# Optimization experiments

Measured on AMD Instinct MI355X. Metric: run time of the kernel, lower is better.

The kernel has to match this reference:

```python
import jax, jax.numpy as jnp
import numpy as np

N = 50000        # num nodes
E = 800000       # num edges (avg degree 16)
IN_DIM = 64
OUT_DIM = 64
PE_DIM = 24
HEADS = 2
HID = OUT_DIM * HEADS  # 128


def setup_inputs() -> dict:
    key = jax.random.key(0)
    ks = jax.random.split(key, 16)
    std = 0.1  # trunc_normal_(std=0.1) init in the torch module
    return {
        "x": jax.random.normal(ks[0], (N, IN_DIM), jnp.float32),
        "pe_index": jax.random.randint(ks[1], (2, E), 0, N, jnp.int32),
        "pe_val": jax.random.normal(ks[2], (E, PE_DIM), jnp.float32),
        # edge-weight MLP (blocks): input proj, one residual FFN block, final proj
        "W_in": jax.random.normal(ks[3], (PE_DIM, HID), jnp.float32) * std,
        "b_in": jnp.zeros((HID,), jnp.float32),
        "W1": jax.random.normal(ks[4], (HID, HID), jnp.float32) * std,
        "b1": jnp.zeros((HID,), jnp.float32),
        "W2": jax.random.normal(ks[5], (HID, HID), jnp.float32) * std,
        "b2": jnp.zeros((HID,), jnp.float32),
        "W_fin": jax.random.normal(ks[6], (HID, HID), jnp.float32) * std,
        "b_fin": jnp.zeros((HID,), jnp.float32),
        # node feature -> multi-head projection
        "W_x": jax.random.normal(ks[7], (IN_DIM, HID), jnp.float32) * std,
        "b_x": jnp.zeros((HID,), jnp.float32),
        # per-head output bias
        "head_bias": jnp.zeros((1, HEADS, OUT_DIM), jnp.float32),
        # final out projection
        "W_out": jax.random.normal(ks[8], (HID, OUT_DIM), jnp.float32) * std,
        "b_out": jnp.zeros((OUT_DIM,), jnp.float32),
    }


def _edge_mlp(pe, W_in, b_in, W1, b1, W2, b2, W_fin, b_fin):
    # Linear(pe_dim->hid), then residual block [GELU, Linear, GELU, Linear, +res], then Linear(hid->hid)
    g = lambda t: jax.nn.gelu(t, approximate=False)  # torch nn.GELU default = exact erf
    x0 = pe @ W_in + b_in                     # [E, HID]
    h = g(x0) @ W1 + b1
    h = g(h) @ W2 + b2
    x0 = h + x0                               # ResidualLayer: x + x_res
    return x0 @ W_fin + b_fin                 # [E, HID]


def reference(x, pe_index, pe_val, W_in, b_in, W1, b1, W2, b2, W_fin, b_fin,
              W_x, b_x, head_bias, W_out, b_out):
    tgt = pe_index[0]  # messages aggregate to edge_index[0]
    src = pe_index[1]
    score = _edge_mlp(pe_val, W_in, b_in, W1, b1, W2, b2, W_fin, b_fin)
    score = score.reshape(-1, HEADS, OUT_DIM)                 # [E, H, D]
    xh = (x @ W_x + b_x).reshape(-1, HEADS, OUT_DIM)          # [N, H, D]
    msg = xh[src] * score                                     # gather-multiply
    wV = jax.ops.segment_sum(msg, tgt, num_segments=N)        # scatter-add [N, H, D]
    deg = jax.ops.segment_sum(jnp.ones((msg.shape[0],), jnp.float32), tgt, num_segments=N)
    wV = wV / jnp.maximum(deg, 1.0)[:, None, None]            # average=True -> mean aggregation
    h = (wV + head_bias).reshape(-1, HEADS * OUT_DIM)
    return h @ W_out + b_out                                  # out_proj: [N, OUT_DIM]
```

## Files before the change

### kernel.cpp

```cpp
#include <hip/hip_runtime.h>
#include <hip/hip_bf16.h>
#include <math.h>

#define NN 50000
#define EE 800000
#define HID 128
#define PED 24
#define IND 64
#define OUTD 64
#define EBLK 128
#define AKS 136

typedef short bf16x8 __attribute__((ext_vector_type(8)));
typedef float f32x4 __attribute__((ext_vector_type(4)));

__device__ __forceinline__ float gelu_fast(float x) {
    float x2 = x * x;
    float t = __builtin_fmaf(x2, -0.07135481627f, -1.5957691216f);
    float e = __expf(x * t);
    return x * __builtin_amdgcn_rcpf(1.0f + e);
}
__device__ __forceinline__ unsigned short f2bf(float f) {
    unsigned int u = __float_as_uint(f);
    u = (u + 0x7fffu + ((u >> 16) & 1u)) >> 16;
    return (unsigned short)u;
}
__device__ __forceinline__ unsigned int pkbf2(float a, float b) {
    __hip_bfloat162 h = __float22bfloat162_rn(make_float2(a, b));
    return *reinterpret_cast<unsigned int*>(&h);
}
__device__ __forceinline__ float bf2f(unsigned short u) {
    return __uint_as_float((unsigned int)u << 16);
}

__global__ __launch_bounds__(256) void pre_kernel(
    const float* __restrict__ x, const float* __restrict__ W_x,
    const float* __restrict__ b_x, unsigned short* __restrict__ xhb,
    const float* __restrict__ W_in, const float* __restrict__ W1,
    const float* __restrict__ W2, const float* __restrict__ Wf,
    unsigned short* __restrict__ WT_in, unsigned short* __restrict__ WT1,
    unsigned short* __restrict__ WT2, unsigned short* __restrict__ WTf,
    float* __restrict__ wV, int* __restrict__ cnt) {
    int bx = blockIdx.x;
    if (bx < 6250) {
        int gid = bx * 256 + threadIdx.x;
        int n = gid >> 5;
        int q = gid & 31;
        *(float4*)&wV[(size_t)n * HID + q * 4] = make_float4(0.f, 0.f, 0.f, 0.f);
        const float* xr = x + (size_t)n * IND;
        float4 acc = *(const float4*)&b_x[q * 4];
#pragma unroll 8
        for (int k = 0; k < IND; k++) {
            float xk = xr[k];
            float4 w = *(const float4*)&W_x[k * HID + q * 4];
            acc.x += xk * w.x; acc.y += xk * w.y;
            acc.z += xk * w.z; acc.w += xk * w.w;
        }
        uint2 p;
        p.x = pkbf2(acc.x, acc.y);
        p.y = pkbf2(acc.z, acc.w);
        ((uint2*)&xhb[(size_t)n * HID])[q] = p;
    } else {
        int idx = (bx - 6250) * 256 + threadIdx.x;
        if (idx < NN) cnt[idx] = 0;
        if (idx < 4096) {
            int j = idx >> 5, k = idx & 31;
            WT_in[idx] = f2bf(k < PED ? W_in[k * HID + j] : 0.f);
        } else if (idx < 4096 + 16384) {
            int i = idx - 4096; int j = i >> 7, k = i & 127;
            WT1[i] = f2bf(W1[k * HID + j]);
        } else if (idx < 4096 + 32768) {
            int i = idx - 4096 - 16384; int j = i >> 7, k = i & 127;
            WT2[i] = f2bf(W2[k * HID + j]);
        } else if (idx < 4096 + 49152) {
            int i = idx - 4096 - 32768; int j = i >> 7, k = i & 127;
            WTf[i] = f2bf(Wf[k * HID + j]);
        }
    }
}

__global__ __launch_bounds__(256) void hist_kernel(const int* __restrict__ pe_idx,
                                                   int* __restrict__ cnt) {
    int e = blockIdx.x * 256 + threadIdx.x;
    if (e < EE) atomicAdd(&cnt[pe_idx[e]], 1);
}

__global__ __launch_bounds__(1024) void scan_kernel(const int* __restrict__ cnt,
                                                    int* __restrict__ woff) {
    __shared__ int s_w[16];
    int tid = threadIdx.x;
    const int chunk = (NN + 1023) / 1024;
    int base = tid * chunk;
    int end = base + chunk; if (end > NN) end = NN;
    int s = 0;
    for (int i = base; i < end; i++) s += cnt[i];
    int v = s;
    int lane = tid & 63, wid = tid >> 6;
#pragma unroll
    for (int d = 1; d < 64; d <<= 1) {
        int u = __shfl_up(v, d, 64);
        if (lane >= d) v += u;
    }
    if (lane == 63) s_w[wid] = v;
    __syncthreads();
    if (tid < 16) {
        int wv = s_w[tid];
#pragma unroll
        for (int d = 1; d < 16; d <<= 1) {
            int u = __shfl_up(wv, d, 64);
            if (tid >= d) wv += u;
        }
        s_w[tid] = wv;
    }
    __syncthreads();
    int exc = v - s + (wid ? s_w[wid - 1] : 0);
    int run = exc;
    for (int i = base; i < end; i++) { woff[i] = run; run += cnt[i]; }
}

__global__ __launch_bounds__(256) void scatter_kernel(const int* __restrict__ pe_idx,
                                                      int* __restrict__ woff,
                                                      int* __restrict__ perm) {
    int e = blockIdx.x * 256 + threadIdx.x;
    if (e < EE) {
        int t = pe_idx[e];
        int p = atomicAdd(&woff[t], 1);
        perm[p] = e;
    }
}

__global__ __launch_bounds__(512, 4) void edge_kernel(
    const float* __restrict__ pe_val, const int* __restrict__ pe_idx,
    const int* __restrict__ perm, const unsigned short* __restrict__ xhb,
    const unsigned short* __restrict__ WT_in, const unsigned short* __restrict__ WT1,
    const unsigned short* __restrict__ WT2, const unsigned short* __restrict__ WTf,
    const float* __restrict__ b_in, const float* __restrict__ b1,
    const float* __restrict__ b2, const float* __restrict__ bfin,
    float* __restrict__ wV) {
    __shared__ __align__(16) unsigned short s_act[2][EBLK][AKS];
    __shared__ int s_tgt[EBLK], s_src[EBLK];

    const int tid = threadIdx.x;
    const int lane = tid & 63;
    const int w = tid >> 6;
    const int cg = w & 3;
    const int eh = w >> 2;
    const int ebase = eh * 64;
    const int l15 = lane & 15;
    const int quad = lane >> 4;
    const long b0 = (long)blockIdx.x * EBLK;

    if (tid < EBLK) {
        int eid = perm[b0 + tid];
        s_tgt[tid] = pe_idx[eid];
        s_src[tid] = pe_idx[EE + eid];
    }
#pragma unroll
    for (int i = 0; i < 4; i++) {
        int idx = tid + i * 512; int e = idx >> 4, k2 = idx & 15;
        float2 v = make_float2(0.f, 0.f);
        if (k2 < 12) {
            int eid = perm[b0 + e];
            v = *(const float2*)&pe_val[(size_t)eid * PED + k2 * 2];
        }
        *(unsigned int*)&s_act[0][e][k2 * 2] = pkbf2(v.x, v.y);
    }
    __syncthreads();

    f32x4 C[2][4];
    f32x4 x0s[2][4];

    {
        float4 ba = *(const float4*)&b_in[(2 * cg + 0) * 16 + quad * 4];
        float4 bb = *(const float4*)&b_in[(2 * cg + 1) * 16 + quad * 4];
        f32x4 ci0 = {ba.x, ba.y, ba.z, ba.w};
        f32x4 ci1 = {bb.x, bb.y, bb.z, bb.w};
        bf16x8 a0 = *(const bf16x8*)&WT_in[((2 * cg + 0) * 16 + l15) * 32 + quad * 8];
        bf16x8 a1 = *(const bf16x8*)&WT_in[((2 * cg + 1) * 16 + l15) * 32 + quad * 8];
#pragma unroll
        for (int u = 0; u < 4; u++) {
            bf16x8 bfr = *(const bf16x8*)&s_act[0][ebase + u * 16 + l15][quad * 8];
            C[0][u] = __builtin_amdgcn_mfma_f32_16x16x32_bf16(a0, bfr, ci0, 0, 0, 0);
            C[1][u] = __builtin_amdgcn_mfma_f32_16x16x32_bf16(a1, bfr, ci1, 0, 0, 0);
        }
    }
#pragma unroll
    for (int t = 0; t < 2; t++) {
        int ch0 = (2 * cg + t) * 16 + quad * 4;
#pragma unroll
        for (int u = 0; u < 4; u++) {
            int e = ebase + u * 16 + l15;
            f32x4 c = C[t][u];
            x0s[t][u] = c;
            uint2 p;
            p.x = pkbf2(gelu_fast(c[0]), gelu_fast(c[1]));
            p.y = pkbf2(gelu_fast(c[2]), gelu_fast(c[3]));
            *(uint2*)&s_act[1][e][ch0] = p;
        }
    }
    __syncthreads();

#define GEMM128(WT, BIAS, SB)                                                  \
    {                                                                          \
        float4 ba_ = *(const float4*)&(BIAS)[(2 * cg + 0) * 16 + quad * 4];    \
        float4 bb_ = *(const float4*)&(BIAS)[(2 * cg + 1) * 16 + quad * 4];    \
        f32x4 ci0 = {ba_.x, ba_.y, ba_.z, ba_.w};                              \
        f32x4 ci1 = {bb_.x, bb_.y, bb_.z, bb_.w};                              \
        _Pragma("unroll") for (int u = 0; u < 4; u++) {                        \
            C[0][u] = ci0; C[1][u] = ci1;                                      \
        }                                                                      \
        _Pragma("unroll") for (int ks = 0; ks < 4; ks++) {                     \
            bf16x8 a0 = *(const bf16x8*)&(WT)[((2 * cg + 0) * 16 + l15) * HID  \
                                              + ks * 32 + quad * 8];           \
            bf16x8 a1 = *(const bf16x8*)&(WT)[((2 * cg + 1) * 16 + l15) * HID  \
                                              + ks * 32 + quad * 8];           \
            _Pragma("unroll") for (int u = 0; u < 4; u++) {                    \
                bf16x8 bfr = *(const bf16x8*)&s_act[SB][ebase + u * 16 + l15]  \
                                                   [ks * 32 + quad * 8];       \
                C[0][u] = __builtin_amdgcn_mfma_f32_16x16x32_bf16(a0, bfr,     \
                                                                  C[0][u], 0, 0, 0); \
                C[1][u] = __builtin_amdgcn_mfma_f32_16x16x32_bf16(a1, bfr,     \
                                                                  C[1][u], 0, 0, 0); \
            }                                                                  \
        }                                                                      \
    }

    GEMM128(WT1, b1, 1);
#pragma unroll
    for (int t = 0; t < 2; t++) {
        int ch0 = (2 * cg + t) * 16 + quad * 4;
#pragma unroll
        for (int u = 0; u < 4; u++) {
            int e = ebase + u * 16 + l15;
            f32x4 c = C[t][u];
            uint2 p;
            p.x = pkbf2(gelu_fast(c[0]), gelu_fast(c[1]));
            p.y = pkbf2(gelu_fast(c[2]), gelu_fast(c[3]));
            *(uint2*)&s_act[0][e][ch0] = p;
        }
    }
    __syncthreads();

    GEMM128(WT2, b2, 0);
#pragma unroll
    for (int t = 0; t < 2; t++) {
        int ch0 = (2 * cg + t) * 16 + quad * 4;
#pragma unroll
        for (int u = 0; u < 4; u++) {
            int e = ebase + u * 16 + l15;
            f32x4 c = C[t][u];
            f32x4 x0 = x0s[t][u];
            uint2 p;
            p.x = pkbf2(c[0] + x0[0], c[1] + x0[1]);
            p.y = pkbf2(c[2] + x0[2], c[3] + x0[3]);
            *(uint2*)&s_act[1][e][ch0] = p;
        }
    }
    __syncthreads();

    GEMM128(WTf, bfin, 1);
#pragma unroll
    for (int t = 0; t < 2; t++) {
        int ch0 = (2 * cg + t) * 16 + quad * 4;
#pragma unroll
        for (int u = 0; u < 4; u++) {
            int e = ebase + u * 16 + l15;
            f32x4 c = C[t][u];
            uint2 p;
            p.x = pkbf2(c[0], c[1]);
            p.y = pkbf2(c[2], c[3]);
            *(uint2*)&s_act[0][e][ch0] = p;
        }
    }
    __syncthreads();

    {
        const int c = tid & 127;
        const int q = tid >> 7;
        const int e0 = q * 32;
        float acc = 0.f;
        int prev = s_tgt[e0];
        bool firstseg = true;
#pragma unroll
        for (int b = 0; b < 4; b++) {
            float xs[8];
#pragma unroll
            for (int j = 0; j < 8; j++) {
                int e = e0 + b * 8 + j;
                xs[j] = bf2f(xhb[(size_t)s_src[e] * HID + c]);
            }
#pragma unroll
            for (int j = 0; j < 8; j++) {
                int e = e0 + b * 8 + j;
                int tg = s_tgt[e];
                if (tg != prev) {
                    if (firstseg) atomicAdd(&wV[(size_t)prev * HID + c], acc);
                    else          wV[(size_t)prev * HID + c] = acc;
                    firstseg = false;
                    acc = 0.f;
                    prev = tg;
                }
                float sc = bf2f(s_act[0][e][c]);
                acc += xs[j] * sc;
            }
        }
        atomicAdd(&wV[(size_t)prev * HID + c], acc);
    }
#undef GEMM128
}

__global__ __launch_bounds__(256) void out_kernel(
    const float* __restrict__ wV, const int* __restrict__ cnt,
    const float* __restrict__ head_bias, const float* __restrict__ W_out,
    const float* __restrict__ b_out, float* __restrict__ out) {
    int gid = blockIdx.x * 256 + threadIdx.x;
    int n = gid >> 4;
    int q = gid & 15;
    if (n >= NN) return;
    float inv = 1.0f / fmaxf((float)cnt[n], 1.0f);
    const float* wr = wV + (size_t)n * HID;
    float4 acc = *(const float4*)&b_out[q * 4];
#pragma unroll 4
    for (int k = 0; k < HID; k++) {
        float hv = wr[k] * inv + head_bias[k];
        float4 wv4 = *(const float4*)&W_out[k * OUTD + q * 4];
        acc.x += hv * wv4.x; acc.y += hv * wv4.y;
        acc.z += hv * wv4.z; acc.w += hv * wv4.w;
    }
    *(float4*)&out[(size_t)n * OUTD + q * 4] = acc;
}

extern "C" void kernel_launch(void* const* d_in, const int* in_sizes, int n_in,
                              void* d_out, int out_size, void* d_ws, size_t ws_size,
                              hipStream_t stream) {
    const float* x      = (const float*)d_in[0];
    const int*   pe_idx = (const int*)d_in[1];
    const float* pe_val = (const float*)d_in[2];
    const float* W_in   = (const float*)d_in[3];
    const float* b_in   = (const float*)d_in[4];
    const float* W1     = (const float*)d_in[5];
    const float* b1     = (const float*)d_in[6];
    const float* W2     = (const float*)d_in[7];
    const float* b2     = (const float*)d_in[8];
    const float* Wf     = (const float*)d_in[9];
    const float* bfin   = (const float*)d_in[10];
    const float* W_x    = (const float*)d_in[11];
    const float* b_x    = (const float*)d_in[12];
    const float* hb     = (const float*)d_in[13];
    const float* W_out  = (const float*)d_in[14];
    const float* b_out  = (const float*)d_in[15];
    float* out = (float*)d_out;

    float* wV   = (float*)d_ws;
    int*   cnt  = (int*)(wV + (size_t)NN * HID);
    int*   woff = cnt + NN;
    int*   perm = woff + NN;
    unsigned short* WT_in = (unsigned short*)(perm + EE);
    unsigned short* WT1   = WT_in + 128 * 32;
    unsigned short* WT2   = WT1 + 128 * 128;
    unsigned short* WTf   = WT2 + 128 * 128;
    unsigned short* xhb   = WTf + 128 * 128;

    pre_kernel<<<6250 + 208, 256, 0, stream>>>(x, W_x, b_x, xhb,
                                               W_in, W1, W2, Wf,
                                               WT_in, WT1, WT2, WTf, wV, cnt);
    hist_kernel<<<(EE + 255) / 256, 256, 0, stream>>>(pe_idx, cnt);
    scan_kernel<<<1, 1024, 0, stream>>>(cnt, woff);
    scatter_kernel<<<(EE + 255) / 256, 256, 0, stream>>>(pe_idx, woff, perm);

    edge_kernel<<<EE / EBLK, 512, 0, stream>>>(pe_val, pe_idx, perm, xhb,
                                               WT_in, WT1, WT2, WTf,
                                               b_in, b1, b2, bfin, wV);

    out_kernel<<<(NN * 16 + 255) / 256, 256, 0, stream>>>(wV, cnt, hb, W_out,
                                                          b_out, out);
}
```

Before: 702.3 us.

## Restructure edge MLP kernel: smaller edge tile, LDS-staged swizzled weights, vectorized scatter

Shrinks the edge tile from 128 to 80 edges and drops the double-buffered padded activation array for a single XOR-swizzled activation buffer. Each 128x128 weight matrix is now staged once into LDS with the same swizzle, so waves read MFMA A fragments from shared memory instead of global memory. The residual x0 is kept packed in bf16, and the xh gathers are issued before the final sync. The scatter step now handles 4 channels per thread with 5 edges per group and always uses atomics. Occupancy is raised to 6 blocks per CU, at the cost of more barriers, more weight-staging traffic per edge, and more atomics per edge.

```diff
diff --git a/kernel.cpp b/kernel.cpp
--- a/kernel.cpp
+++ b/kernel.cpp
@@ -8,8 +8,7 @@
 #define PED 24
 #define IND 64
 #define OUTD 64
-#define EBLK 128
-#define AKS 136
+#define EBLK 80
 
 typedef short bf16x8 __attribute__((ext_vector_type(8)));
 typedef float f32x4 __attribute__((ext_vector_type(4)));
@@ -29,8 +28,11 @@
     __hip_bfloat162 h = __float22bfloat162_rn(make_float2(a, b));
     return *reinterpret_cast<unsigned int*>(&h);
 }
-__device__ __forceinline__ float bf2f(unsigned short u) {
-    return __uint_as_float((unsigned int)u << 16);
+__device__ __forceinline__ float bflo(unsigned int u) {
+    return __uint_as_float(u << 16);
+}
+__device__ __forceinline__ float bfhi(unsigned int u) {
+    return __uint_as_float(u & 0xffff0000u);
 }
 
 __global__ __launch_bounds__(256) void pre_kernel(
@@ -129,7 +131,7 @@
     }
 }
 
-__global__ __launch_bounds__(512, 4) void edge_kernel(
+__global__ __launch_bounds__(512, 6) void edge_kernel(
     const float* __restrict__ pe_val, const int* __restrict__ pe_idx,
     const int* __restrict__ perm, const unsigned short* __restrict__ xhb,
     const unsigned short* __restrict__ WT_in, const unsigned short* __restrict__ WT1,
@@ -137,18 +139,19 @@
     const float* __restrict__ b_in, const float* __restrict__ b1,
     const float* __restrict__ b2, const float* __restrict__ bfin,
     float* __restrict__ wV) {
-    __shared__ __align__(16) unsigned short s_act[2][EBLK][AKS];
+    __shared__ __align__(16) unsigned short s_W[HID * HID];
+    __shared__ __align__(16) unsigned short s_act[EBLK * HID];
     __shared__ int s_tgt[EBLK], s_src[EBLK];
 
     const int tid = threadIdx.x;
     const int lane = tid & 63;
-    const int w = tid >> 6;
-    const int cg = w & 3;
-    const int eh = w >> 2;
-    const int ebase = eh * 64;
+    const int cg = tid >> 6;
     const int l15 = lane & 15;
     const int quad = lane >> 4;
+    const int swz4 = (l15 & 7) << 4;
     const long b0 = (long)blockIdx.x * EBLK;
+    char* actB = (char*)s_act;
+    char* wB = (char*)s_W;
 
     if (tid < EBLK) {
         int eid = perm[b0 + tid];
@@ -157,156 +160,154 @@
     }
 #pragma unroll
     for (int i = 0; i < 4; i++) {
-        int idx = tid + i * 512; int e = idx >> 4, k2 = idx & 15;
-        float2 v = make_float2(0.f, 0.f);
-        if (k2 < 12) {
-            int eid = perm[b0 + e];
-            v = *(const float2*)&pe_val[(size_t)eid * PED + k2 * 2];
-        }
-        *(unsigned int*)&s_act[0][e][k2 * 2] = pkbf2(v.x, v.y);
-    }
-    __syncthreads();
-
-    f32x4 C[2][4];
-    f32x4 x0s[2][4];
+        int idx = tid + i * 512; int r = idx >> 4, seg = idx & 15;
+        *(uint4*)(wB + r * 256 + ((seg * 16) ^ ((r & 7) << 4))) =
+            *(const uint4*)&WT1[r * HID + seg * 8];
+    }
+#pragma unroll
+    for (int i = 0; i < 3; i++) {
+        int idx = tid + i * 512;
+        if (idx < EBLK * 16) {
+            int e = idx >> 4, k2 = idx & 15;
+            float2 v = make_float2(0.f, 0.f);
+            if (k2 < 12) {
+                int eid = perm[b0 + e];
+                v = *(const float2*)&pe_val[(size_t)eid * PED + k2 * 2];
+            }
+            *(unsigned int*)(actB + e * 256 + ((k2 * 4) ^ ((e & 7) << 4))) =
+                pkbf2(v.x, v.y);
+        }
+    }
+    __syncthreads();
+
+    const int ch0 = cg * 16 + quad * 4;
+    f32x4 C[5];
+    unsigned int x0pk[5][2];
 
     {
-        float4 ba = *(const float4*)&b_in[(2 * cg + 0) * 16 + quad * 4];
-        float4 bb = *(const float4*)&b_in[(2 * cg + 1) * 16 + quad * 4];
-        f32x4 ci0 = {ba.x, ba.y, ba.z, ba.w};
-        f32x4 ci1 = {bb.x, bb.y, bb.z, bb.w};
-        bf16x8 a0 = *(const bf16x8*)&WT_in[((2 * cg + 0) * 16 + l15) * 32 + quad * 8];
-        bf16x8 a1 = *(const bf16x8*)&WT_in[((2 * cg + 1) * 16 + l15) * 32 + quad * 8];
-#pragma unroll
-        for (int u = 0; u < 4; u++) {
-            bf16x8 bfr = *(const bf16x8*)&s_act[0][ebase + u * 16 + l15][quad * 8];
-            C[0][u] = __builtin_amdgcn_mfma_f32_16x16x32_bf16(a0, bfr, ci0, 0, 0, 0);
-            C[1][u] = __builtin_amdgcn_mfma_f32_16x16x32_bf16(a1, bfr, ci1, 0, 0, 0);
-        }
-    }
-#pragma unroll
-    for (int t = 0; t < 2; t++) {
-        int ch0 = (2 * cg + t) * 16 + quad * 4;
-#pragma unroll
-        for (int u = 0; u < 4; u++) {
-            int e = ebase + u * 16 + l15;
-            f32x4 c = C[t][u];
-            x0s[t][u] = c;
-            uint2 p;
-            p.x = pkbf2(gelu_fast(c[0]), gelu_fast(c[1]));
-            p.y = pkbf2(gelu_fast(c[2]), gelu_fast(c[3]));
-            *(uint2*)&s_act[1][e][ch0] = p;
-        }
-    }
-    __syncthreads();
-
-#define GEMM128(WT, BIAS, SB)                                                  \
+        float4 bb = *(const float4*)&b_in[ch0];
+        f32x4 ci = {bb.x, bb.y, bb.z, bb.w};
+        bf16x8 a = *(const bf16x8*)&WT_in[(cg * 16 + l15) * 32 + quad * 8];
+#pragma unroll
+        for (int u = 0; u < 5; u++) {
+            bf16x8 bfr = *(const bf16x8*)(actB + (u * 16 + l15) * 256 +
+                                          ((quad * 16) ^ swz4));
+            C[u] = __builtin_amdgcn_mfma_f32_16x16x32_bf16(a, bfr, ci, 0, 0, 0);
+        }
+    }
+    __syncthreads();
+#pragma unroll
+    for (int u = 0; u < 5; u++) {
+        int e = u * 16 + l15;
+        f32x4 c = C[u];
+        x0pk[u][0] = pkbf2(c[0], c[1]);
+        x0pk[u][1] = pkbf2(c[2], c[3]);
+        uint2 p;
+        p.x = pkbf2(gelu_fast(c[0]), gelu_fast(c[1]));
+        p.y = pkbf2(gelu_fast(c[2]), gelu_fast(c[3]));
+        *(uint2*)(actB + e * 256 + ((ch0 * 2) ^ swz4)) = p;
+    }
+    __syncthreads();
+
+#define GEMM128(BIAS)                                                          \
     {                                                                          \
-        float4 ba_ = *(const float4*)&(BIAS)[(2 * cg + 0) * 16 + quad * 4];    \
-        float4 bb_ = *(const float4*)&(BIAS)[(2 * cg + 1) * 16 + quad * 4];    \
-        f32x4 ci0 = {ba_.x, ba_.y, ba_.z, ba_.w};                              \
-        f32x4 ci1 = {bb_.x, bb_.y, bb_.z, bb_.w};                              \
-        _Pragma("unroll") for (int u = 0; u < 4; u++) {                        \
-            C[0][u] = ci0; C[1][u] = ci1;                                      \
-        }                                                                      \
+        float4 bb_ = *(const float4*)&(BIAS)[ch0];                             \
+        f32x4 ci = {bb_.x, bb_.y, bb_.z, bb_.w};                               \
+        _Pragma("unroll") for (int u = 0; u < 5; u++) C[u] = ci;               \
         _Pragma("unroll") for (int ks = 0; ks < 4; ks++) {                     \
-            bf16x8 a0 = *(const bf16x8*)&(WT)[((2 * cg + 0) * 16 + l15) * HID  \
-                                              + ks * 32 + quad * 8];           \
-            bf16x8 a1 = *(const bf16x8*)&(WT)[((2 * cg + 1) * 16 + l15) * HID  \
-                                              + ks * 32 + quad * 8];           \
-            _Pragma("unroll") for (int u = 0; u < 4; u++) {                    \
-                bf16x8 bfr = *(const bf16x8*)&s_act[SB][ebase + u * 16 + l15]  \
-                                                   [ks * 32 + quad * 8];       \
-                C[0][u] = __builtin_amdgcn_mfma_f32_16x16x32_bf16(a0, bfr,     \
-                                                                  C[0][u], 0, 0, 0); \
-                C[1][u] = __builtin_amdgcn_mfma_f32_16x16x32_bf16(a1, bfr,     \
-                                                                  C[1][u], 0, 0, 0); \
+            bf16x8 a = *(const bf16x8*)(wB + (cg * 16 + l15) * 256 +           \
+                                        ((ks * 64 + quad * 16) ^ swz4));       \
+            _Pragma("unroll") for (int u = 0; u < 5; u++) {                    \
+                bf16x8 bfr = *(const bf16x8*)(actB + (u * 16 + l15) * 256 +    \
+                                              ((ks * 64 + quad * 16) ^ swz4)); \
+                C[u] = __builtin_amdgcn_mfma_f32_16x16x32_bf16(a, bfr, C[u],   \
+                                                               0, 0, 0);       \
             }                                                                  \
         }                                                                      \
     }
 
-    GEMM128(WT1, b1, 1);
-#pragma unroll
-    for (int t = 0; t < 2; t++) {
-        int ch0 = (2 * cg + t) * 16 + quad * 4;
-#pragma unroll
-        for (int u = 0; u < 4; u++) {
-            int e = ebase + u * 16 + l15;
-            f32x4 c = C[t][u];
-            uint2 p;
-            p.x = pkbf2(gelu_fast(c[0]), gelu_fast(c[1]));
-            p.y = pkbf2(gelu_fast(c[2]), gelu_fast(c[3]));
-            *(uint2*)&s_act[0][e][ch0] = p;
-        }
-    }
-    __syncthreads();
-
-    GEMM128(WT2, b2, 0);
-#pragma unroll
-    for (int t = 0; t < 2; t++) {
-        int ch0 = (2 * cg + t) * 16 + quad * 4;
-#pragma unroll
-        for (int u = 0; u < 4; u++) {
-            int e = ebase + u * 16 + l15;
-            f32x4 c = C[t][u];
-            f32x4 x0 = x0s[t][u];
-            uint2 p;
-            p.x = pkbf2(c[0] + x0[0], c[1] + x0[1]);
-            p.y = pkbf2(c[2] + x0[2], c[3] + x0[3]);
-            *(uint2*)&s_act[1][e][ch0] = p;
-        }
-    }
-    __syncthreads();
-
-    GEMM128(WTf, bfin, 1);
-#pragma unroll
-    for (int t = 0; t < 2; t++) {
-        int ch0 = (2 * cg + t) * 16 + quad * 4;
-#pragma unroll
-        for (int u = 0; u < 4; u++) {
-            int e = ebase + u * 16 + l15;
-            f32x4 c = C[t][u];
-            uint2 p;
-            p.x = pkbf2(c[0], c[1]);
-            p.y = pkbf2(c[2], c[3]);
-            *(uint2*)&s_act[0][e][ch0] = p;
-        }
+#define STAGE_W(WT)                                                            \
+    _Pragma("unroll") for (int i = 0; i < 4; i++) {                            \
+        int idx = tid + i * 512; int r = idx >> 4, seg = idx & 15;             \
+        *(uint4*)(wB + r * 256 + ((seg * 16) ^ ((r & 7) << 4))) =              \
+            *(const uint4*)&(WT)[r * HID + seg * 8];                           \
+    }
+
+    GEMM128(b1);
+    __syncthreads();
+#pragma unroll
+    for (int u = 0; u < 5; u++) {
+        int e = u * 16 + l15;
+        f32x4 c = C[u];
+        uint2 p;
+        p.x = pkbf2(gelu_fast(c[0]), gelu_fast(c[1]));
+        p.y = pkbf2(gelu_fast(c[2]), gelu_fast(c[3]));
+        *(uint2*)(actB + e * 256 + ((ch0 * 2) ^ swz4)) = p;
+    }
+    STAGE_W(WT2);
+    __syncthreads();
+
+    GEMM128(b2);
+    __syncthreads();
+#pragma unroll
+    for (int u = 0; u < 5; u++) {
+        int e = u * 16 + l15;
+        f32x4 c = C[u];
+        uint2 p;
+        p.x = pkbf2(c[0] + bflo(x0pk[u][0]), c[1] + bfhi(x0pk[u][0]));
+        p.y = pkbf2(c[2] + bflo(x0pk[u][1]), c[3] + bfhi(x0pk[u][1]));
+        *(uint2*)(actB + e * 256 + ((ch0 * 2) ^ swz4)) = p;
+    }
+    STAGE_W(WTf);
+    __syncthreads();
+
+    GEMM128(bfin);
+    const int g = tid >> 5;
+    const int c4w = tid & 31;
+    uint2 xv[5];
+#pragma unroll
+    for (int j = 0; j < 5; j++) {
+        xv[j] = *(const uint2*)&xhb[(size_t)s_src[g * 5 + j] * HID + c4w * 4];
+    }
+    __syncthreads();
+#pragma unroll
+    for (int u = 0; u < 5; u++) {
+        int e = u * 16 + l15;
+        f32x4 c = C[u];
+        uint2 p;
+        p.x = pkbf2(c[0], c[1]);
+        p.y = pkbf2(c[2], c[3]);
+        *(uint2*)(actB + e * 256 + ((ch0 * 2) ^ swz4)) = p;
     }
     __syncthreads();
 
     {
-        const int c = tid & 127;
-        const int q = tid >> 7;
-        const int e0 = q * 32;
-        float acc = 0.f;
-        int prev = s_tgt[e0];
-        bool firstseg = true;
-#pragma unroll
-        for (int b = 0; b < 4; b++) {
-            float xs[8];
-#pragma unroll
-            for (int j = 0; j < 8; j++) {
-                int e = e0 + b * 8 + j;
-                xs[j] = bf2f(xhb[(size_t)s_src[e] * HID + c]);
+        float a0 = 0.f, a1 = 0.f, a2 = 0.f, a3 = 0.f;
+        int prev = s_tgt[g * 5];
+#pragma unroll
+        for (int j = 0; j < 5; j++) {
+            int e = g * 5 + j;
+            int tg = s_tgt[e];
+            uint2 sc = *(const uint2*)(actB + e * 256 +
+                                       ((c4w * 8) ^ ((e & 7) << 4)));
+            if (tg != prev) {
+                float* wp = &wV[(size_t)prev * HID + c4w * 4];
+                atomicAdd(wp + 0, a0); atomicAdd(wp + 1, a1);
+                atomicAdd(wp + 2, a2); atomicAdd(wp + 3, a3);
+                a0 = a1 = a2 = a3 = 0.f;
+                prev = tg;
             }
-#pragma unroll
-            for (int j = 0; j < 8; j++) {
-                int e = e0 + b * 8 + j;
-                int tg = s_tgt[e];
-                if (tg != prev) {
-                    if (firstseg) atomicAdd(&wV[(size_t)prev * HID + c], acc);
-                    else          wV[(size_t)prev * HID + c] = acc;
-                    firstseg = false;
-                    acc = 0.f;
-                    prev = tg;
-                }
-                float sc = bf2f(s_act[0][e][c]);
-                acc += xs[j] * sc;
-            }
-        }
-        atomicAdd(&wV[(size_t)prev * HID + c], acc);
+            a0 += bflo(xv[j].x) * bflo(sc.x);
+            a1 += bfhi(xv[j].x) * bfhi(sc.x);
+            a2 += bflo(xv[j].y) * bflo(sc.y);
+            a3 += bfhi(xv[j].y) * bfhi(sc.y);
+        }
+        float* wp = &wV[(size_t)prev * HID + c4w * 4];
+        atomicAdd(wp + 0, a0); atomicAdd(wp + 1, a1);
+        atomicAdd(wp + 2, a2); atomicAdd(wp + 3, a3);
     }
 #undef GEMM128
+#undef STAGE_W
 }
 
 __global__ __launch_bounds__(256) void out_kernel(
```

Measured after the change: 848.4 us. 1.21x slower.
